# Kernel optimization log

Hardware: AMD Instinct MI355X
Metric: run time of the kernel (lower is better)

Reference implementation:

```python
import jax, jax.numpy as jnp
import numpy as np

B, S, H, E, V = 32, 256, 512, 300, 32000
ALEN, LLEN, POL = 4, 16, 3
HOP, LAM = 10, 0.01


def _layernorm(x, g, b, eps=1e-12):
    mu = jnp.mean(x, -1, keepdims=True)
    var = jnp.mean((x - mu) ** 2, -1, keepdims=True)
    return (x - mu) / jnp.sqrt(var + eps) * g + b


def _pos_weight(x, a0, a1, text_len, aspect_len):
    # vectorized version of ASGCN_NEW.position_weight
    j = jnp.arange(x.shape[1])[None, :]
    cl = (text_len - aspect_len).astype(jnp.float32)[:, None]
    a0b, a1b, tlb = a0[:, None], a1[:, None], text_len[:, None]
    w = jnp.where(j < a0b, 1.0 - (a0b - j) / cl,
        jnp.where(j <= a1b, 0.0,
        jnp.where(j < tlb, 1.0 - (j - a1b) / cl, 0.0)))
    return w[:, :, None] * x


def _mask(x, a0, a1):
    j = jnp.arange(x.shape[1])[None, :]
    m = ((j >= a0[:, None]) & (j <= a1[:, None])).astype(x.dtype)
    return m[:, :, None] * x


def _gcn(x, adj, w, b):
    h = jnp.einsum('bsh,hk->bsk', x, w)
    denom = jnp.sum(adj, 2, keepdims=True) + 1.0
    return jnp.einsum('bst,bth->bsh', adj, h) / denom + b


def _conv1d(x, w, b):
    # x: [B,S,C] -> conv over S with kernel 3, pad 1 -> [B,S,C]
    y = jax.lax.conv_general_dilated(jnp.swapaxes(x, 1, 2), w, (1,), ((1, 1),),
                                     dimension_numbers=('NCH', 'OIH', 'NCH'))
    return jnp.swapaxes(y + b[None, :, None], 1, 2)


def _lstm_dir(x, mask, wih, whh, b, reverse):
    # masked LSTM matching pack_padded semantics: state frozen / output zero at pad
    xs = jnp.swapaxes(x, 0, 1)       # [S,B,E]
    ms = jnp.swapaxes(mask, 0, 1)    # [S,B] bool
    if reverse:
        xs, ms = xs[::-1], ms[::-1]
    pre = jnp.einsum('sbe,ge->sbg', xs, wih) + b
    h0 = jnp.zeros((x.shape[0], whh.shape[1]), x.dtype)

    def step(carry, inp):
        h, c = carry
        p, m = inp
        g = p + h @ whh.T
        i, f, gg, o = jnp.split(g, 4, -1)
        c_new = jax.nn.sigmoid(f) * c + jax.nn.sigmoid(i) * jnp.tanh(gg)
        h_new = jax.nn.sigmoid(o) * jnp.tanh(c_new)
        m_ = m[:, None]
        return (jnp.where(m_, h_new, h), jnp.where(m_, c_new, c)), jnp.where(m_, h_new, 0.0)

    _, ys = jax.lax.scan(step, (h0, h0), (pre, ms))
    if reverse:
        ys = ys[::-1]
    return jnp.swapaxes(ys, 0, 1)


def _hop_attend(m, text_out, g, b):
    tT = jnp.swapaxes(text_out, 1, 2)
    for _ in range(HOP - 1):
        alpha = jnp.einsum('bsh,bht->bst', m, tT)          # [B,S,S]
        a = jnp.einsum('bst,bth->bsh', alpha, text_out)    # [B,S,H]
        m = LAM * _layernorm(jax.nn.sigmoid(a), g, b) + m
    alpha_mat = jnp.einsum('bsh,bht->bst', m, tT)
    alpha = jax.nn.softmax(jnp.sum(alpha_mat, 1, keepdims=True), axis=2)  # [B,1,S]
    return jnp.einsum('bot,bth->boh', alpha, text_out)[:, 0]              # [B,H]


def setup_inputs() -> dict:
    key = jax.random.key(0)
    ks = jax.random.split(key, 20)
    sc = 0.05
    text_indices = jax.random.randint(ks[0], (B, S), 1, V)
    aspect_indices = jax.random.randint(ks[1], (B, ALEN), 1, V)
    left_indices = jax.random.randint(ks[2], (B, LLEN), 1, V)
    adj = (jax.random.uniform(ks[3], (B, S, S)) < 0.1).astype(jnp.float32)
    adj = jnp.minimum(adj + jnp.eye(S, dtype=jnp.float32)[None], 1.0)
    return {
        'text_indices': text_indices,
        'aspect_indices': aspect_indices,
        'left_indices': left_indices,
        'adj': adj,
        'embedding': jax.random.normal(ks[4], (V, E)) * sc,
        'lstm_wih_f': jax.random.normal(ks[5], (4 * H, E)) * sc,
        'lstm_whh_f': jax.random.normal(ks[6], (4 * H, H)) * sc,
        'lstm_b_f': jnp.zeros((4 * H,), jnp.float32),
        'lstm_wih_b': jax.random.normal(ks[7], (4 * H, E)) * sc,
        'lstm_whh_b': jax.random.normal(ks[8], (4 * H, H)) * sc,
        'lstm_b_b': jnp.zeros((4 * H,), jnp.float32),
        'gc_w': jax.random.normal(ks[9], (6, H, H)) * sc,
        'gc_b': jnp.zeros((6, H), jnp.float32),
        'conv1_w': jax.random.normal(ks[10], (H, H, 3)) * sc,
        'conv1_b': jnp.zeros((H,), jnp.float32),
        'conv2_w': jax.random.normal(ks[11], (H, H, 3)) * sc,
        'conv2_b': jnp.zeros((H,), jnp.float32),
        'fc2_w': jax.random.normal(ks[12], (POL, 3 * H)) * sc,
        'fc2_b': jnp.zeros((POL,), jnp.float32),
        'ln_g': jnp.ones((3, H), jnp.float32),
        'ln_b': jnp.zeros((3, H), jnp.float32),
    }


def _forward(text_indices, aspect_indices, left_indices, adj, embedding,
             lstm_wih_f, lstm_whh_f, lstm_b_f, lstm_wih_b, lstm_whh_b, lstm_b_b,
             gc_w, gc_b, conv1_w, conv1_b, conv2_w, conv2_b, fc2_w, fc2_b, ln_g, ln_b):
    text_len = jnp.sum(text_indices != 0, -1)
    aspect_len = jnp.sum(aspect_indices != 0, -1)
    left_len = jnp.sum(left_indices != 0, -1)
    a0 = left_len
    a1 = left_len + aspect_len - 1
    text = embedding[text_indices]  # dropout identity in eval mode
    m = text_indices != 0
    hf = _lstm_dir(text, m, lstm_wih_f, lstm_whh_f, lstm_b_f, False)
    hb = _lstm_dir(text, m, lstm_wih_b, lstm_whh_b, lstm_b_b, True)
    # concat fwd/bwd then reshape(B,S,H,2).mean(-1), exactly as the torch code
    text_out = jnp.concatenate([hf, hb], -1).reshape(B, S, H, 2).mean(-1)

    pw = lambda t: _pos_weight(t, a0, a1, text_len, aspect_len)

    x_conv = jax.nn.relu(_conv1d(pw(text_out), conv1_w, conv1_b))
    x_conv = jax.nn.relu(_conv1d(pw(x_conv), conv2_w, conv2_b))

    x = jax.nn.relu(_gcn(pw(text_out), adj, gc_w[0], gc_b[0]))
    pwx = pw(x)
    graph_mask = jnp.zeros_like(x)
    for k in range(1, 6):
        graph_mask = graph_mask + _mask(jax.nn.relu(_gcn(pwx, adj, gc_w[k], gc_b[k])), a0, a1)

    a1_vec = _hop_attend(graph_mask, text_out, ln_g[0], ln_b[0])
    a2_vec = _hop_attend(_mask(text_out, a0, a1), text_out, ln_g[1], ln_b[1])
    a3_vec = _hop_attend(_mask(x_conv, a0, a1), text_out, ln_g[2], ln_b[2])

    fnout = jnp.concatenate([a1_vec, a2_vec, a3_vec], 1)  # [B, 3H]
    return fnout @ fc2_w.T + fc2_b


def reference(text_indices, aspect_indices, left_indices, adj, embedding,
              lstm_wih_f, lstm_whh_f, lstm_b_f, lstm_wih_b, lstm_whh_b, lstm_b_b,
              gc_w, gc_b, conv1_w, conv1_b, conv2_w, conv2_b, fc2_w, fc2_b, ln_g, ln_b):
    return _forward(text_indices, aspect_indices, left_indices, adj, embedding,
                    lstm_wih_f, lstm_whh_f, lstm_b_f, lstm_wih_b, lstm_whh_b, lstm_b_b,
                    gc_w, gc_b, conv1_w, conv1_b, conv2_w, conv2_b, fc2_w, fc2_b, ln_g, ln_b)
```

## Files before the change

kernel.cpp:

```cpp
#include <hip/hip_runtime.h>
#include <hip/hip_fp16.h>

typedef unsigned int u32;
typedef unsigned long long u64;

static constexpr size_t OFF_X2    = 0;
static constexpr size_t OFF_PRE   = 9830400;
static constexpr size_t OFF_MB    = 131072;
static constexpr size_t OFF_CNT   = 133120;
static constexpr size_t OFF_TOUT  = 0;
static constexpr size_t OFF_TOUTT = 16777216;
static constexpr size_t OFF_PWT   = 33554432;
static constexpr size_t OFF_AGG0  = 50331648;
static constexpr size_t OFF_Y     = 76939264;
static constexpr size_t OFF_PWX   = 110493696;
static constexpr size_t OFF_WD    = 127270912;
static constexpr size_t OFF_WIH   = 131465216;
static constexpr size_t OFF_BIA   = 136380416;
static constexpr size_t OFF_W1T   = 136396800;
static constexpr size_t OFF_W2T   = 139542528;
static constexpr size_t OFF_META  = 142688256;
static constexpr size_t OFF_CLF   = 142688768;
static constexpr size_t OFF_DEN   = 142688896;
static constexpr size_t OFF_POSW  = 142721664;
static constexpr size_t OFF_AGGM  = 142754432;
static constexpr size_t OFF_GMSK  = 143016576;
static constexpr size_t OFF_C1PW  = 143278720;
static constexpr size_t OFF_XC2   = 143671936;
static constexpr size_t OFF_AVEC  = 143934080;
static constexpr size_t WS_NEED   = 144130688;

__device__ __forceinline__ float sigf(float x) { return 1.f / (1.f + expf(-x)); }

typedef _Float16 half8 __attribute__((ext_vector_type(8)));
typedef float f32x4 __attribute__((ext_vector_type(4)));
union U4H8 { uint4 u; half8 h; };

__global__ void len_k(const int* __restrict__ ti, const int* __restrict__ ai,
                      const int* __restrict__ li, int* __restrict__ meta, float* __restrict__ clf)
{
    int b = threadIdx.x;
    if (b >= 32) return;
    int tl = 0;
    for (int s = 0; s < 256; ++s) tl += (ti[b*256+s] != 0);
    int al = 0;
    for (int i = 0; i < 4; ++i) al += (ai[b*4+i] != 0);
    int ll = 0;
    for (int i = 0; i < 16; ++i) ll += (li[b*16+i] != 0);
    meta[b]      = ll;
    meta[32+b]   = ll + al - 1;
    meta[64+b]   = al;
    meta[96+b]   = tl;
    clf[b] = (float)(tl - al);
}

__global__ __launch_bounds__(256)
void pd_k(const float* __restrict__ adj, const int* __restrict__ meta,
          const float* __restrict__ clf, float* __restrict__ denom, float* __restrict__ posw)
{
    int row = blockIdx.x;
    int b = row >> 8, s = row & 255;
    int tid = threadIdx.x;
    float v = adj[(size_t)row*256 + tid];
    #pragma unroll
    for (int off = 1; off < 64; off <<= 1) v += __shfl_xor(v, off);
    __shared__ float rd[4];
    if ((tid & 63) == 0) rd[tid >> 6] = v;
    __syncthreads();
    if (tid == 0) {
        denom[row] = rd[0] + rd[1] + rd[2] + rd[3] + 1.f;
        int a0 = meta[b], a1 = meta[32+b], tl = meta[96+b];
        float cl = clf[b];
        float w;
        if (s < a0)       w = 1.f - (float)(a0 - s) / cl;
        else if (s <= a1) w = 0.f;
        else if (s < tl)  w = 1.f - (float)(s - a1) / cl;
        else              w = 0.f;
        posw[row] = w;
    }
}

__global__ __launch_bounds__(128)
void gather_k(const int* __restrict__ ti, const float* __restrict__ emb, __half* __restrict__ X2h)
{
    int row = blockIdx.x;
    int b = row & 31, s = row >> 5;
    int idx = ti[b*256 + s];
    const float* e = emb + (size_t)idx*300;
    __half* o = X2h + (size_t)row*320;
    for (int k = threadIdx.x; k < 320; k += 128)
        o[k] = (k < 300) ? __float2half(e[k]) : __ushort_as_half((unsigned short)0);
}

__global__ __launch_bounds__(256)
void wpackih_k(const float* __restrict__ wf, const float* __restrict__ wb, u32* __restrict__ Wih)
{
    u32 idx = blockIdx.x*256 + threadIdx.x;
    if (idx >= 655360u) return;
    int n = idx / 160;
    int j = idx - n*160;
    int k0 = 2*j;
    const float* w = (n < 2048) ? (wf + (size_t)n*300) : (wb + (size_t)(n - 2048)*300);
    float v0 = (k0   < 300) ? w[k0]   : 0.f;
    float v1 = (k0+1 < 300) ? w[k0+1] : 0.f;
    Wih[idx] = (u32)__half_as_ushort(__float2half(v0)) |
               ((u32)__half_as_ushort(__float2half(v1)) << 16);
}

__global__ __launch_bounds__(256)
void wmf_k(const float* __restrict__ wf, const float* __restrict__ wb, u32* __restrict__ Wmf)
{
    u32 idx = blockIdx.x*256 + threadIdx.x;
    int e2 = idx & 3;
    int l  = (idx >> 2) & 63;
    int c  = (idx >> 8) & 3;
    int mt = (idx >> 10) & 1;
    int wv = (idx >> 11) & 3;
    int g  = (idx >> 13) & 63;
    int dir = (int)(idx >> 19);
    int kloc = wv*128 + c*32 + 16*(e2 >> 1) + 4*(l >> 4) + 2*(e2 & 1);
    int ml = mt*16 + (l & 15);
    int n = (ml & 3)*512 + g*8 + (ml >> 2);
    const float* w = dir ? wb : wf;
    float v0 = w[(size_t)n*512 + kloc];
    float v1 = w[(size_t)n*512 + kloc + 1];
    Wmf[idx] = (u32)__half_as_ushort(__float2half(v0)) |
               ((u32)__half_as_ushort(__float2half(v1)) << 16);
}

__global__ void maskb_k(const int* __restrict__ ti, u32* __restrict__ mb)
{
    int s = threadIdx.x;
    u32 w = 0;
    for (int b = 0; b < 32; ++b) w |= (u32)(ti[b*256 + s] != 0) << b;
    mb[s] = w;
}

__global__ __launch_bounds__(256)
void wtrans_k(const float* __restrict__ w1, const float* __restrict__ w2,
              float* __restrict__ w1T, float* __restrict__ w2T)
{
    u32 idx = blockIdx.x*256 + threadIdx.x;
    const float* src = blockIdx.y ? w2 : w1;
    float* dst = blockIdx.y ? w2T : w1T;
    int k = idx >> 18;
    int i = (idx >> 9) & 511;
    int o = idx & 511;
    dst[idx] = src[((size_t)o*512 + i)*3 + k];
}

__global__ __launch_bounds__(256)
void pre_mfma_k(const u32* __restrict__ X2u, const u32* __restrict__ Wihu,
                const float* __restrict__ bias, __half* __restrict__ pre)
{
    __shared__ u32 As2[16*132];
    __shared__ u32 Bs2[16*132];
    const int tid = threadIdx.x;
    const int wv = tid >> 6;
    const int l  = tid & 63;
    const int q  = l >> 4;
    const int l15 = l & 15;
    const int wm = wv & 1, wn = wv >> 1;
    const int m0 = blockIdx.x * 128;
    const int n0 = blockIdx.y * 128;

    f32x4 acc[4][4];
    #pragma unroll
    for (int mt = 0; mt < 4; ++mt)
        #pragma unroll
        for (int nt = 0; nt < 4; ++nt)
            acc[mt][nt] = (f32x4){0.f, 0.f, 0.f, 0.f};

    const int srow = tid >> 4;
    const int sj   = tid & 15;

    for (int kb = 0; kb < 10; ++kb) {
        #pragma unroll
        for (int i = 0; i < 8; ++i) {
            int row = srow + i*16;
            As2[sj*132 + row] = X2u[(size_t)(m0 + row)*160 + kb*16 + sj];
            Bs2[sj*132 + row] = Wihu[(size_t)(n0 + row)*160 + kb*16 + sj];
        }
        __syncthreads();

        U4H8 bf[4];
        #pragma unroll
        for (int nt = 0; nt < 4; ++nt) {
            int col = wn*64 + nt*16 + l15;
            bf[nt].u = make_uint4(Bs2[(2*q)*132 + col], Bs2[(2*q+1)*132 + col],
                                  Bs2[(2*q+8)*132 + col], Bs2[(2*q+9)*132 + col]);
        }
        #pragma unroll
        for (int mt = 0; mt < 4; ++mt) {
            int row = wm*64 + mt*16 + l15;
            U4H8 af;
            af.u = make_uint4(As2[(2*q)*132 + row], As2[(2*q+1)*132 + row],
                              As2[(2*q+8)*132 + row], As2[(2*q+9)*132 + row]);
            #pragma unroll
            for (int nt = 0; nt < 4; ++nt)
                acc[mt][nt] = __builtin_amdgcn_mfma_f32_16x16x32_f16(af.h, bf[nt].h, acc[mt][nt], 0, 0, 0);
        }
        __syncthreads();
    }

    #pragma unroll
    for (int nt = 0; nt < 4; ++nt) {
        int col = n0 + wn*64 + nt*16 + l15;
        float bv = bias[col];
        #pragma unroll
        for (int mt = 0; mt < 4; ++mt) {
            int rbase = m0 + wm*64 + mt*16 + q*4;
            #pragma unroll
            for (int p = 0; p < 4; ++p)
                pre[(size_t)(rbase + p)*4096 + col] = __float2half(acc[mt][nt][p] + bv);
        }
    }
}

__global__ __launch_bounds__(256, 1)
void lstm_scan5_k(const __half* __restrict__ pre, const u32* __restrict__ Wmf,
                  const u32* __restrict__ mb, float* __restrict__ y,
                  u32* __restrict__ cnt, u64* __restrict__ Hs)
{
    __shared__ u32 hs[32*264];
    __shared__ float gred[4352];

    const int tid = threadIdx.x;
    const int wv = tid >> 6;
    const int l  = tid & 63;
    const int q  = l >> 4;
    const int l15 = l & 15;
    const int dir = blockIdx.x & 1;
    const int g   = blockIdx.x >> 1;
    const int b2 = tid >> 3;
    const int jj = tid & 7;
    const int gcol = g*8 + jj;

    half8 afr[2][4];
    {
        const uint4* wp = (const uint4*)(Wmf + ((((size_t)dir*64 + g)*4 + wv)*2048)) + l;
        #pragma unroll
        for (int mt = 0; mt < 2; ++mt)
            #pragma unroll
            for (int c = 0; c < 4; ++c)
                afr[mt][c] = __builtin_bit_cast(half8, wp[(mt*4 + c)*64]);
    }

    float hreg = 0.f, creg = 0.f;

    const int s0 = dir ? 255 : 0;
    __half ph[4];
    #pragma unroll
    for (int gt = 0; gt < 4; ++gt)
        ph[gt] = pre[((size_t)s0*32 + b2)*4096 + dir*2048 + gt*512 + gcol];
    u32 mbv = mb[s0];

    const int ks64 = wv*64;
    const int srow = tid >> 3, scol = tid & 7;

    for (int t = 0; t < 256; ++t) {
        const int s = dir ? (255 - t) : t;

        __half phn[4];
        #pragma unroll
        for (int gt = 0; gt < 4; ++gt) phn[gt] = ph[gt];
        u32 mbn = mbv;
        if (t < 255) {
            int sn = dir ? (254 - t) : (t + 1);
            #pragma unroll
            for (int gt = 0; gt < 4; ++gt)
                phn[gt] = pre[((size_t)sn*32 + b2)*4096 + dir*2048 + gt*512 + gcol];
            mbn = mb[sn];
        }

        if (t == 0) {
            u32* dst = &hs[srow*264 + scol*4];
            #pragma unroll
            for (int i = 0; i < 8; ++i) *(uint4*)(dst + i*32) = make_uint4(0u,0u,0u,0u);
        } else {
            if (tid == 0) {
                const u32* cpp = cnt + (size_t)t*2 + dir;
                int guard = 0;
                while (__hip_atomic_load(cpp, __ATOMIC_RELAXED, __HIP_MEMORY_SCOPE_AGENT) < 64u) {
                    __builtin_amdgcn_s_sleep(2);
                    if (++guard > (1 << 22)) break;
                }
            }
            __syncthreads();
            int bi = (int)(__brev((u32)t) >> 24);
            const uint4* src = (const uint4*)(Hs + ((size_t)(bi*2 + dir)*32)*128);
            const uint4* tp = src + srow*64 + scol;
            uint4 vv[8];
            #pragma unroll
            for (int i = 0; i < 8; ++i) vv[i] = tp[i*8];
            u32* dst = &hs[srow*264 + scol*4];
            #pragma unroll
            for (int i = 0; i < 8; ++i) *(uint4*)(dst + i*32) = vv[i];
        }
        __syncthreads();

        f32x4 acc[2][2];
        #pragma unroll
        for (int mt = 0; mt < 2; ++mt)
            #pragma unroll
            for (int nt = 0; nt < 2; ++nt)
                acc[mt][nt] = (f32x4){0.f, 0.f, 0.f, 0.f};
        #pragma unroll
        for (int c = 0; c < 4; ++c) {
            #pragma unroll
            for (int nt = 0; nt < 2; ++nt) {
                int base = (nt*16 + l15)*264 + ks64 + c*16 + 2*q;
                uint4 bw = make_uint4(hs[base], hs[base+1], hs[base+8], hs[base+9]);
                half8 bfr = __builtin_bit_cast(half8, bw);
                acc[0][nt] = __builtin_amdgcn_mfma_f32_16x16x32_f16(afr[0][c], bfr, acc[0][nt], 0, 0, 0);
                acc[1][nt] = __builtin_amdgcn_mfma_f32_16x16x32_f16(afr[1][c], bfr, acc[1][nt], 0, 0, 0);
            }
        }

        #pragma unroll
        for (int mt = 0; mt < 2; ++mt)
            #pragma unroll
            for (int nt = 0; nt < 2; ++nt)
                #pragma unroll
                for (int p = 0; p < 4; ++p)
                    gred[(((wv*2 + mt)*2 + nt)*16 + q*4 + p)*17 + l15] = acc[mt][nt][p];
        __syncthreads();

        float gv[4];
        #pragma unroll
        for (int gt = 0; gt < 4; ++gt) {
            int ml = 4*jj + gt;
            int mt = ml >> 4, r = ml & 15;
            int ntile = b2 >> 4, n = b2 & 15;
            float sum = 0.f;
            #pragma unroll
            for (int w2 = 0; w2 < 4; ++w2)
                sum += gred[(((w2*2 + mt)*2 + ntile)*16 + r)*17 + n];
            gv[gt] = sum + __half2float(ph[gt]);
        }
        float cn = sigf(gv[1])*creg + sigf(gv[0])*tanhf(gv[2]);
        float hn = sigf(gv[3])*tanhf(cn);
        bool mk = (mbv >> b2) & 1u;
        if (mk) { hreg = hn; creg = cn; }

        {
            int l4 = l & ~3;
            float h0 = __shfl(hreg, l4 + 0);
            float h1 = __shfl(hreg, l4 + 1);
            float h2 = __shfl(hreg, l4 + 2);
            float h3 = __shfl(hreg, l4 + 3);
            if ((tid & 3) == 0) {
                u32 lo = (u32)__half_as_ushort(__float2half(h0)) |
                         ((u32)__half_as_ushort(__float2half(h1)) << 16);
                u32 hi = (u32)__half_as_ushort(__float2half(h2)) |
                         ((u32)__half_as_ushort(__float2half(h3)) << 16);
                u64 pk = (u64)lo | ((u64)hi << 32);
                int bi2 = (int)(__brev((u32)(t + 1)) >> 24);
                int wsel = (tid >> 2) & 1;
                __hip_atomic_store(&Hs[((size_t)(bi2*2 + dir)*32 + b2)*128 + 2*g + wsel], pk,
                                   __ATOMIC_RELAXED, __HIP_MEMORY_SCOPE_AGENT);
            }
        }
        asm volatile("s_waitcnt vmcnt(0)" ::: "memory");
        __syncthreads();
        if (tid == 0) {
            __hip_atomic_fetch_add(cnt + (size_t)(t + 1)*2 + dir, 1u,
                                   __ATOMIC_RELAXED, __HIP_MEMORY_SCOPE_AGENT);
        }
        y[(((size_t)dir*32 + b2)*256 + s)*512 + gcol] = mk ? hn : 0.f;

        mbv = mbn;
        #pragma unroll
        for (int gt = 0; gt < 4; ++gt) ph[gt] = phn[gt];
    }
}

__global__ __launch_bounds__(256)
void combine_k(const float* __restrict__ y, const float* __restrict__ posw,
               float* __restrict__ text_out, float* __restrict__ pw_text)
{
    size_t idx = (size_t)blockIdx.x*256 + threadIdx.x;
    int hh = (int)(idx & 511);
    size_t rem = idx >> 9;
    int s = (int)(rem & 255);
    int b = (int)(rem >> 8);
    const float* p;
    if (hh < 256) p = y + (((size_t)b*256 + s)*512 + 2*hh);
    else          p = y + (((size_t)(32 + b)*256 + s)*512 + 2*(hh - 256));
    float v = 0.5f*(p[0] + p[1]);
    text_out[idx] = v;
    pw_text[idx] = v * posw[b*256 + s];
}

__global__ __launch_bounds__(256)
void transp_k(const float* __restrict__ text_out, float* __restrict__ tOutT)
{
    __shared__ float tile[32][33];
    int b = blockIdx.z, s0 = blockIdx.x*32, h0 = blockIdx.y*32;
    int tx = threadIdx.x & 31, ty4 = threadIdx.x >> 5;
    #pragma unroll
    for (int rr = 0; rr < 4; ++rr) {
        int sy = ty4 + rr*8;
        tile[sy][tx] = text_out[((size_t)b*256 + s0 + sy)*512 + h0 + tx];
    }
    __syncthreads();
    #pragma unroll
    for (int rr = 0; rr < 4; ++rr) {
        int hy = ty4 + rr*8;
        tOutT[((size_t)b*512 + h0 + hy)*256 + s0 + tx] = tile[tx][hy];
    }
}

template<int MODE, bool BT>
__global__ __launch_bounds__(256)
void gemm_k(const float* __restrict__ A, const float* __restrict__ B,
            void* __restrict__ C, int M, int N, int K,
            long sA, long sB, long sC,
            const float* __restrict__ bias,
            const float* __restrict__ denom,
            const float* __restrict__ posw)
{
    __shared__ float As[32][132];
    __shared__ float Bs[32][132];
    const int z = blockIdx.z;
    A += (size_t)z * sA;
    B += (size_t)z * sB;
    const int m0 = blockIdx.x * 128;
    const int n0 = blockIdx.y * 128;
    const int tid = threadIdx.x;
    const int tx = tid & 15, ty = tid >> 4;
    float acc[8][8];
    #pragma unroll
    for (int i = 0; i < 8; ++i)
        #pragma unroll
        for (int j = 0; j < 8; ++j) acc[i][j] = 0.f;
    const int nkb = (K + 31) >> 5;
    for (int kb = 0; kb < nkb; ++kb) {
        const int k0 = kb << 5;
        #pragma unroll
        for (int rep = 0; rep < 4; ++rep) {
            int idx = rep*256 + tid;
            int row = idx >> 3;
            int c4 = (idx & 7) << 2;
            int gk = k0 + c4;
            const float* ap = A + (size_t)(m0 + row)*K + gk;
            float4 v;
            if (gk + 3 < K) v = *(const float4*)ap;
            else {
                v.x = (gk   < K) ? ap[0] : 0.f;
                v.y = (gk+1 < K) ? ap[1] : 0.f;
                v.z = (gk+2 < K) ? ap[2] : 0.f;
                v.w = (gk+3 < K) ? ap[3] : 0.f;
            }
            As[c4+0][row] = v.x; As[c4+1][row] = v.y;
            As[c4+2][row] = v.z; As[c4+3][row] = v.w;
        }
        if (BT) {
            #pragma unroll
            for (int rep = 0; rep < 4; ++rep) {
                int idx = rep*256 + tid;
                int row = idx >> 3;
                int c4 = (idx & 7) << 2;
                int gk = k0 + c4;
                const float* bp = B + (size_t)(n0 + row)*K + gk;
                float4 v;
                if (gk + 3 < K) v = *(const float4*)bp;
                else {
                    v.x = (gk   < K) ? bp[0] : 0.f;
                    v.y = (gk+1 < K) ? bp[1] : 0.f;
                    v.z = (gk+2 < K) ? bp[2] : 0.f;
                    v.w = (gk+3 < K) ? bp[3] : 0.f;
                }
                Bs[c4+0][row] = v.x; Bs[c4+1][row] = v.y;
                Bs[c4+2][row] = v.z; Bs[c4+3][row] = v.w;
            }
        } else {
            #pragma unroll
            for (int rep = 0; rep < 4; ++rep) {
                int idx = rep*256 + tid;
                int kk = idx >> 5;
                int nn = (idx & 31) << 2;
                int gk = k0 + kk;
                float4 v = make_float4(0.f, 0.f, 0.f, 0.f);
                if (gk < K) v = *(const float4*)(B + (size_t)gk*N + n0 + nn);
                *(float4*)&Bs[kk][nn] = v;
            }
        }
        __syncthreads();
        #pragma unroll
        for (int k = 0; k < 32; ++k) {
            float a[8], br[8];
            *(float4*)&a[0]  = *(const float4*)&As[k][ty*8];
            *(float4*)&a[4]  = *(const float4*)&As[k][ty*8+4];
            *(float4*)&br[0] = *(const float4*)&Bs[k][tx*8];
            *(float4*)&br[4] = *(const float4*)&Bs[k][tx*8+4];
            #pragma unroll
            for (int i = 0; i < 8; ++i)
                #pragma unroll
                for (int j = 0; j < 8; ++j)
                    acc[i][j] = fmaf(a[i], br[j], acc[i][j]);
        }
        __syncthreads();
    }
    if (MODE == 1) {
        float* cp = (float*)C + (size_t)z*sC;
        #pragma unroll
        for (int i = 0; i < 8; ++i) {
            size_t ro = (size_t)(m0 + ty*8 + i)*N + n0 + tx*8;
            *(float4*)(cp + ro)     = make_float4(acc[i][0], acc[i][1], acc[i][2], acc[i][3]);
            *(float4*)(cp + ro + 4) = make_float4(acc[i][4], acc[i][5], acc[i][6], acc[i][7]);
        }
    } else {
        float* cp = (float*)C + (size_t)z*sC;
        #pragma unroll
        for (int i = 0; i < 8; ++i) {
            int m = m0 + ty*8 + i;
            float inv = 1.f / denom[m];
            float pw = posw[m];
            size_t ro = (size_t)m*N + n0 + tx*8;
            #pragma unroll
            for (int j = 0; j < 8; ++j) {
                float v = fmaf(acc[i][j], inv, bias[n0 + tx*8 + j]);
                cp[ro + j] = fmaxf(v, 0.f) * pw;
            }
        }
    }
}

__global__ __launch_bounds__(256)
void aggm_k(const float* __restrict__ adj, const float* __restrict__ pwx,
            const int* __restrict__ meta, float* __restrict__ aggm)
{
    int b = blockIdx.x >> 2, r = blockIdx.x & 3;
    int a0 = meta[b], nm = meta[64+b];
    int s = a0 + r; if (s > 255) s = 255;
    __shared__ float arow[256];
    int tid = threadIdx.x;
    arow[tid] = adj[((size_t)b*256 + s)*256 + tid];
    __syncthreads();
    float acc0 = 0.f, acc1 = 0.f;
    for (int t = 0; t < 256; ++t) {
        float av = arow[t];
        acc0 = fmaf(av, pwx[((size_t)b*256 + t)*512 + tid], acc0);
        acc1 = fmaf(av, pwx[((size_t)b*256 + t)*512 + tid + 256], acc1);
    }
    bool ok = (r < nm);
    aggm[((size_t)b*4 + r)*512 + tid]       = ok ? acc0 : 0.f;
    aggm[((size_t)b*4 + r)*512 + tid + 256] = ok ? acc1 : 0.f;
}

__global__ __launch_bounds__(256)
void gmaskn_k(const float* __restrict__ aggm, const float* __restrict__ gcw,
              const float* __restrict__ gcb, const int* __restrict__ meta,
              const float* __restrict__ denom, float* __restrict__ gmsk)
{
    int b = blockIdx.x >> 1, hf = blockIdx.x & 1;
    int col = hf*256 + threadIdx.x;
    int a0 = meta[b], nm = meta[64+b];
    __shared__ float rows[4][512];
    int tid = threadIdx.x;
    #pragma unroll
    for (int r = 0; r < 4; ++r) {
        rows[r][tid]       = aggm[((size_t)b*4 + r)*512 + tid];
        rows[r][tid + 256] = aggm[((size_t)b*4 + r)*512 + tid + 256];
    }
    float inv[4];
    #pragma unroll
    for (int r = 0; r < 4; ++r) {
        int srow = a0 + r; if (srow > 255) srow = 255;
        inv[r] = 1.f / denom[b*256 + srow];
    }
    __syncthreads();
    float gm[4] = {0.f, 0.f, 0.f, 0.f};
    for (int k = 1; k <= 5; ++k) {
        const float* w = gcw + (size_t)k*262144 + col;
        float bb = gcb[k*512 + col];
        float ak[4] = {0.f, 0.f, 0.f, 0.f};
        for (int c = 0; c < 512; ++c) {
            float wv = w[(size_t)c*512];
            #pragma unroll
            for (int r = 0; r < 4; ++r) ak[r] = fmaf(rows[r][c], wv, ak[r]);
        }
        #pragma unroll
        for (int r = 0; r < 4; ++r) gm[r] += fmaxf(fmaf(ak[r], inv[r], bb), 0.f);
    }
    #pragma unroll
    for (int r = 0; r < 4; ++r)
        gmsk[((size_t)b*4 + r)*512 + col] = (r < nm) ? gm[r] : 0.f;
}

__global__ __launch_bounds__(256)
void conv1n_k(const float* __restrict__ pwt, const float* __restrict__ w1T,
              const float* __restrict__ b1, const int* __restrict__ meta,
              const float* __restrict__ posw, float* __restrict__ c1pw)
{
    int b = blockIdx.x >> 1, hf = blockIdx.x & 1;
    int col = hf*256 + threadIdx.x;
    int a0 = meta[b];
    __shared__ float rows[8][512];
    int tid = threadIdx.x;
    #pragma unroll
    for (int i = 0; i < 8; ++i) {
        int si = a0 - 2 + i;
        bool v = (si >= 0 && si < 256);
        rows[i][tid]       = v ? pwt[((size_t)b*256 + si)*512 + tid]       : 0.f;
        rows[i][tid + 256] = v ? pwt[((size_t)b*256 + si)*512 + tid + 256] : 0.f;
    }
    __syncthreads();
    float bv = b1[col];
    float acc[6] = {bv, bv, bv, bv, bv, bv};
    #pragma unroll
    for (int kk = 0; kk < 3; ++kk) {
        const float* w = w1T + (size_t)kk*262144 + col;
        for (int c = 0; c < 512; ++c) {
            float wv = w[(size_t)c*512];
            #pragma unroll
            for (int r = 0; r < 6; ++r) acc[r] = fmaf(rows[r + kk][c], wv, acc[r]);
        }
    }
    #pragma unroll
    for (int r = 0; r < 6; ++r) {
        int s = a0 - 1 + r;
        bool valid = (s >= 0 && s < 256);
        float pv = valid ? posw[b*256 + s] : 0.f;
        c1pw[((size_t)b*6 + r)*512 + col] = valid ? fmaxf(acc[r], 0.f)*pv : 0.f;
    }
}

__global__ __launch_bounds__(256)
void conv2n_k(const float* __restrict__ c1pw, const float* __restrict__ w2T,
              const float* __restrict__ b2, const int* __restrict__ meta,
              float* __restrict__ xc2)
{
    int b = blockIdx.x >> 1, hf = blockIdx.x & 1;
    int col = hf*256 + threadIdx.x;
    int nm = meta[64+b];
    __shared__ float rows[6][512];
    int tid = threadIdx.x;
    #pragma unroll
    for (int i = 0; i < 6; ++i) {
        rows[i][tid]       = c1pw[((size_t)b*6 + i)*512 + tid];
        rows[i][tid + 256] = c1pw[((size_t)b*6 + i)*512 + tid + 256];
    }
    __syncthreads();
    float bv = b2[col];
    float acc[4] = {bv, bv, bv, bv};
    #pragma unroll
    for (int kk = 0; kk < 3; ++kk) {
        const float* w = w2T + (size_t)kk*262144 + col;
        for (int c = 0; c < 512; ++c) {
            float wv = w[(size_t)c*512];
            #pragma unroll
            for (int r = 0; r < 4; ++r) acc[r] = fmaf(rows[r + kk][c], wv, acc[r]);
        }
    }
    #pragma unroll
    for (int r = 0; r < 4; ++r)
        xc2[((size_t)b*4 + r)*512 + col] = (r < nm) ? fmaxf(acc[r], 0.f) : 0.f;
}

__global__ __launch_bounds__(512)
void attend_k(const float* __restrict__ text_out, const float* __restrict__ tOutT,
              const float* __restrict__ gmsk, const float* __restrict__ xc2,
              const int* __restrict__ meta,
              const float* __restrict__ lng, const float* __restrict__ lnb,
              float* __restrict__ avec)
{
    __shared__ float m5[5][512];
    __shared__ float alpha[5][256];
    __shared__ float apart[5][256];
    __shared__ float wt[256];
    __shared__ float msum[512];
    __shared__ float red[8];
    int b = blockIdx.x, att = blockIdx.y;
    int tid = threadIdx.x;
    int a0 = meta[b], nm = meta[64+b];
    #pragma unroll
    for (int r = 0; r < 4; ++r) {
        float v = 0.f;
        if (r < nm) {
            if (att == 0)      v = gmsk[((size_t)b*4 + r)*512 + tid];
            else if (att == 1) v = text_out[((size_t)b*256 + a0 + r)*512 + tid];
            else               v = xc2[((size_t)b*4 + r)*512 + tid];
        }
        m5[r][tid] = v;
    }
    m5[4][tid] = 0.f;
    const float* tT = tOutT + (size_t)b*512*256;
    const float* tO = text_out + (size_t)b*256*512;
    float lgam = lng[att*512 + tid], lbet = lnb[att*512 + tid];
    __syncthreads();
    for (int hop = 0; hop < 9; ++hop) {
        {
            int t = tid & 255, hf = tid >> 8;
            float a5[5] = {0.f, 0.f, 0.f, 0.f, 0.f};
            const float* tp = tT + (size_t)(hf*256)*256 + t;
            for (int h = 0; h < 256; ++h) {
                float v = tp[(size_t)h*256];
                int hh = hf*256 + h;
                #pragma unroll
                for (int r = 0; r < 5; ++r) a5[r] = fmaf(m5[r][hh], v, a5[r]);
            }
            if (hf == 0) { for (int r = 0; r < 5; ++r) alpha[r][t] = a5[r]; }
            else         { for (int r = 0; r < 5; ++r) apart[r][t] = a5[r]; }
        }
        __syncthreads();
        for (int idx = tid; idx < 1280; idx += 512) {
            int r = idx >> 8, t2 = idx & 255;
            alpha[r][t2] += apart[r][t2];
        }
        __syncthreads();
        float a5[5] = {0.f, 0.f, 0.f, 0.f, 0.f};
        for (int t = 0; t < 256; ++t) {
            float v = tO[(size_t)t*512 + tid];
            #pragma unroll
            for (int r = 0; r < 5; ++r) a5[r] = fmaf(alpha[r][t], v, a5[r]);
        }
        #pragma unroll 1
        for (int r = 0; r < 5; ++r) {
            float xv = sigf(a5[r]);
            float s1 = xv;
            #pragma unroll
            for (int off = 1; off < 64; off <<= 1) s1 += __shfl_xor(s1, off);
            if ((tid & 63) == 0) red[tid >> 6] = s1;
            __syncthreads();
            float mu = (red[0]+red[1]+red[2]+red[3]+red[4]+red[5]+red[6]+red[7]) * (1.f/512.f);
            __syncthreads();
            float d = xv - mu;
            float s2 = d*d;
            #pragma unroll
            for (int off = 1; off < 64; off <<= 1) s2 += __shfl_xor(s2, off);
            if ((tid & 63) == 0) red[tid >> 6] = s2;
            __syncthreads();
            float var = (red[0]+red[1]+red[2]+red[3]+red[4]+red[5]+red[6]+red[7]) * (1.f/512.f);
            __syncthreads();
            float ln = d * rsqrtf(var + 1e-12f) * lgam + lbet;
            if (r < nm || r == 4) m5[r][tid] += 0.01f * ln;
        }
        __syncthreads();
    }
    {
        float ms = 0.f;
        #pragma unroll
        for (int r = 0; r < 4; ++r) if (r < nm) ms += m5[r][tid];
        ms += (float)(256 - nm) * m5[4][tid];
        msum[tid] = ms;
    }
    __syncthreads();
    {
        int t = tid & 255, hf = tid >> 8;
        float sc = 0.f;
        const float* tp = tT + (size_t)(hf*256)*256 + t;
        for (int h = 0; h < 256; ++h) sc = fmaf(msum[hf*256 + h], tp[(size_t)h*256], sc);
        if (hf == 0) alpha[0][t] = sc; else apart[0][t] = sc;
    }
    __syncthreads();
    float sv = (tid < 256) ? (alpha[0][tid] + apart[0][tid]) : -3.0e38f;
    float mx = sv;
    #pragma unroll
    for (int off = 1; off < 64; off <<= 1) mx = fmaxf(mx, __shfl_xor(mx, off));
    if ((tid & 63) == 0) red[tid >> 6] = mx;
    __syncthreads();
    mx = fmaxf(fmaxf(fmaxf(red[0], red[1]), fmaxf(red[2], red[3])),
               fmaxf(fmaxf(red[4], red[5]), fmaxf(red[6], red[7])));
    __syncthreads();
    float ex = (tid < 256) ? expf(sv - mx) : 0.f;
    float ss = ex;
    #pragma unroll
    for (int off = 1; off < 64; off <<= 1) ss += __shfl_xor(ss, off);
    if ((tid & 63) == 0) red[tid >> 6] = ss;
    __syncthreads();
    float tot = red[0]+red[1]+red[2]+red[3]+red[4]+red[5]+red[6]+red[7];
    __syncthreads();
    if (tid < 256) wt[tid] = ex / tot;
    __syncthreads();
    float acc = 0.f;
    for (int t = 0; t < 256; ++t) acc = fmaf(wt[t], tO[(size_t)t*512 + tid], acc);
    avec[((size_t)att*32 + b)*512 + tid] = acc;
}

__global__ __launch_bounds__(128)
void final_k(const float* __restrict__ avec, const float* __restrict__ fw,
             const float* __restrict__ fbb, float* __restrict__ out)
{
    int b = blockIdx.x, tid = threadIdx.x;
    float a0 = 0.f, a1 = 0.f, a2 = 0.f;
    for (int j = tid; j < 1536; j += 128) {
        float v = avec[((size_t)(j >> 9)*32 + b)*512 + (j & 511)];
        a0 = fmaf(v, fw[j], a0);
        a1 = fmaf(v, fw[1536 + j], a1);
        a2 = fmaf(v, fw[3072 + j], a2);
    }
    #pragma unroll
    for (int off = 1; off < 64; off <<= 1) {
        a0 += __shfl_xor(a0, off); a1 += __shfl_xor(a1, off); a2 += __shfl_xor(a2, off);
    }
    __shared__ float red[6];
    if ((tid & 63) == 0) { int w = tid >> 6; red[w] = a0; red[2+w] = a1; red[4+w] = a2; }
    __syncthreads();
    if (tid == 0) {
        out[b*3+0] = red[0] + red[1] + fbb[0];
        out[b*3+1] = red[2] + red[3] + fbb[1];
        out[b*3+2] = red[4] + red[5] + fbb[2];
    }
}

extern "C" void kernel_launch(void* const* d_in, const int* in_sizes, int n_in,
                              void* d_out, int out_size, void* d_ws, size_t ws_size,
                              hipStream_t stream)
{
    (void)in_sizes; (void)n_in; (void)out_size;
    if (ws_size < WS_NEED) return;
    const int*   ti    = (const int*)d_in[0];
    const int*   ai    = (const int*)d_in[1];
    const int*   li    = (const int*)d_in[2];
    const float* adj   = (const float*)d_in[3];
    const float* emb   = (const float*)d_in[4];
    const float* wih_f = (const float*)d_in[5];
    const float* whh_f = (const float*)d_in[6];
    const float* b_f   = (const float*)d_in[7];
    const float* wih_b = (const float*)d_in[8];
    const float* whh_b = (const float*)d_in[9];
    const float* b_b   = (const float*)d_in[10];
    const float* gcw   = (const float*)d_in[11];
    const float* gcb   = (const float*)d_in[12];
    const float* c1w   = (const float*)d_in[13];
    const float* c1b   = (const float*)d_in[14];
    const float* c2w   = (const float*)d_in[15];
    const float* c2b   = (const float*)d_in[16];
    const float* fw    = (const float*)d_in[17];
    const float* fb    = (const float*)d_in[18];
    const float* lng   = (const float*)d_in[19];
    const float* lnb   = (const float*)d_in[20];

    char* ws = (char*)d_ws;
    __half* X2h      = (__half*)(ws + OFF_X2);
    __half* pre      = (__half*)(ws + OFF_PRE);
    u32*    mb       = (u32*)(ws + OFF_MB);
    u32*    cnt      = (u32*)(ws + OFF_CNT);
    float*  text_out = (float*)(ws + OFF_TOUT);
    float*  tOutT    = (float*)(ws + OFF_TOUTT);
    float*  pw_text  = (float*)(ws + OFF_PWT);
    float*  agg0     = (float*)(ws + OFF_AGG0);
    float*  y        = (float*)(ws + OFF_Y);
    float*  pwx      = (float*)(ws + OFF_PWX);
    u64*    Hs       = (u64*)(ws + OFF_PWX);
    u32*    Wmf      = (u32*)(ws + OFF_WD);
    u32*    Wih      = (u32*)(ws + OFF_WIH);
    float*  biascat  = (float*)(ws + OFF_BIA);
    float*  w1T      = (float*)(ws + OFF_W1T);
    float*  w2T      = (float*)(ws + OFF_W2T);
    int*    meta     = (int*)(ws + OFF_META);
    float*  clf      = (float*)(ws + OFF_CLF);
    float*  denom    = (float*)(ws + OFF_DEN);
    float*  posw     = (float*)(ws + OFF_POSW);
    float*  aggm     = (float*)(ws + OFF_AGGM);
    float*  gmsk     = (float*)(ws + OFF_GMSK);
    float*  c1pw     = (float*)(ws + OFF_C1PW);
    float*  xc2      = (float*)(ws + OFF_XC2);
    float*  avec     = (float*)(ws + OFF_AVEC);

    len_k<<<1, 64, 0, stream>>>(ti, ai, li, meta, clf);
    pd_k<<<8192, 256, 0, stream>>>(adj, meta, clf, denom, posw);
    gather_k<<<8192, 128, 0, stream>>>(ti, emb, X2h);
    wpackih_k<<<2560, 256, 0, stream>>>(wih_f, wih_b, Wih);
    wmf_k<<<4096, 256, 0, stream>>>(whh_f, whh_b, Wmf);
    wtrans_k<<<dim3(3072, 2), 256, 0, stream>>>(c1w, c2w, w1T, w2T);
    hipMemcpyAsync(biascat,        b_f, 2048*4, hipMemcpyDeviceToDevice, stream);
    hipMemcpyAsync(biascat + 2048, b_b, 2048*4, hipMemcpyDeviceToDevice, stream);

    pre_mfma_k<<<dim3(64, 32), 256, 0, stream>>>((const u32*)X2h, Wih, biascat, pre);

    maskb_k<<<1, 256, 0, stream>>>(ti, mb);
    hipMemsetAsync(cnt, 0, (size_t)257*2*4, stream);

    lstm_scan5_k<<<128, 256, 0, stream>>>(pre, Wmf, mb, y, cnt, Hs);
    combine_k<<<16384, 256, 0, stream>>>(y, posw, text_out, pw_text);
    transp_k<<<dim3(8, 16, 32), 256, 0, stream>>>(text_out, tOutT);

    gemm_k<1, false><<<dim3(2, 4, 32), 256, 0, stream>>>(adj, pw_text, (void*)agg0,
        256, 512, 256, 65536L, 131072L, 131072L, nullptr, nullptr, nullptr);
    gemm_k<2, false><<<dim3(64, 4, 1), 256, 0, stream>>>(agg0, gcw, (void*)pwx,
        8192, 512, 512, 0, 0, 0, gcb, denom, posw);

    aggm_k<<<128, 256, 0, stream>>>(adj, pwx, meta, aggm);
    gmaskn_k<<<64, 256, 0, stream>>>(aggm, gcw, gcb, meta, denom, gmsk);
    conv1n_k<<<64, 256, 0, stream>>>(pw_text, w1T, c1b, meta, posw, c1pw);
    conv2n_k<<<64, 256, 0, stream>>>(c1pw, w2T, c2b, meta, xc2);
    attend_k<<<dim3(32, 3), 512, 0, stream>>>(text_out, tOutT, gmsk, xc2, meta, lng, lnb, avec);
    final_k<<<32, 128, 0, stream>>>(avec, fw, fb, (float*)d_out);
}
```

Measured before the change: 1.734 ms.

## Replace atomic counter barrier with per-block flags polled by a full wavefront

The cross-block step barrier in the LSTM scan now uses one flag per producer block per timestep instead of a single fetch-add counter. Each producer writes its own flag with a plain atomic store, and a whole wavefront of 64 lanes polls the 64 flags, combined with __all. This removes contention from atomic adds on a single word and uses a shorter sleep. The prefetch of the next step's pre-activations and mask moves to the end of the step. That shortens the live range of the prefetched values, but the load overlaps less with the barrier wait. The flag buffer is larger and needs a larger memset.

```diff
diff --git a/kernel.cpp b/kernel.cpp
--- a/kernel.cpp
+++ b/kernel.cpp
@@ -7,7 +7,7 @@
 static constexpr size_t OFF_X2    = 0;
 static constexpr size_t OFF_PRE   = 9830400;
 static constexpr size_t OFF_MB    = 131072;
-static constexpr size_t OFF_CNT   = 133120;
+static constexpr size_t OFF_FLG   = 135168;
 static constexpr size_t OFF_TOUT  = 0;
 static constexpr size_t OFF_TOUTT = 16777216;
 static constexpr size_t OFF_PWT   = 33554432;
@@ -218,9 +218,9 @@
 }
 
 __global__ __launch_bounds__(256, 1)
-void lstm_scan5_k(const __half* __restrict__ pre, const u32* __restrict__ Wmf,
+void lstm_scan6_k(const __half* __restrict__ pre, const u32* __restrict__ Wmf,
                   const u32* __restrict__ mb, float* __restrict__ y,
-                  u32* __restrict__ cnt, u64* __restrict__ Hs)
+                  u32* __restrict__ flags, u64* __restrict__ Hs)
 {
     __shared__ u32 hs[32*264];
     __shared__ float gred[4352];
@@ -261,28 +261,18 @@
     for (int t = 0; t < 256; ++t) {
         const int s = dir ? (255 - t) : t;
 
-        __half phn[4];
-        #pragma unroll
-        for (int gt = 0; gt < 4; ++gt) phn[gt] = ph[gt];
-        u32 mbn = mbv;
-        if (t < 255) {
-            int sn = dir ? (254 - t) : (t + 1);
-            #pragma unroll
-            for (int gt = 0; gt < 4; ++gt)
-                phn[gt] = pre[((size_t)sn*32 + b2)*4096 + dir*2048 + gt*512 + gcol];
-            mbn = mb[sn];
-        }
-
         if (t == 0) {
             u32* dst = &hs[srow*264 + scol*4];
             #pragma unroll
             for (int i = 0; i < 8; ++i) *(uint4*)(dst + i*32) = make_uint4(0u,0u,0u,0u);
         } else {
-            if (tid == 0) {
-                const u32* cpp = cnt + (size_t)t*2 + dir;
+            if (tid < 64) {
+                const u32* fp = flags + (size_t)t*128 + dir*64 + tid;
                 int guard = 0;
-                while (__hip_atomic_load(cpp, __ATOMIC_RELAXED, __HIP_MEMORY_SCOPE_AGENT) < 64u) {
-                    __builtin_amdgcn_s_sleep(2);
+                u32 fv = __hip_atomic_load(fp, __ATOMIC_RELAXED, __HIP_MEMORY_SCOPE_AGENT);
+                while (!__all(fv != 0u)) {
+                    __builtin_amdgcn_s_sleep(1);
+                    fv = __hip_atomic_load(fp, __ATOMIC_RELAXED, __HIP_MEMORY_SCOPE_AGENT);
                     if (++guard > (1 << 22)) break;
                 }
             }
@@ -364,14 +354,18 @@
         asm volatile("s_waitcnt vmcnt(0)" ::: "memory");
         __syncthreads();
         if (tid == 0) {
-            __hip_atomic_fetch_add(cnt + (size_t)(t + 1)*2 + dir, 1u,
-                                   __ATOMIC_RELAXED, __HIP_MEMORY_SCOPE_AGENT);
+            __hip_atomic_store(flags + (size_t)(t + 1)*128 + dir*64 + g, 1u,
+                               __ATOMIC_RELAXED, __HIP_MEMORY_SCOPE_AGENT);
         }
         y[(((size_t)dir*32 + b2)*256 + s)*512 + gcol] = mk ? hn : 0.f;
 
-        mbv = mbn;
-        #pragma unroll
-        for (int gt = 0; gt < 4; ++gt) ph[gt] = phn[gt];
+        if (t < 255) {
+            int sn = dir ? (254 - t) : (t + 1);
+            #pragma unroll
+            for (int gt = 0; gt < 4; ++gt)
+                ph[gt] = pre[((size_t)sn*32 + b2)*4096 + dir*2048 + gt*512 + gcol];
+            mbv = mb[sn];
+        }
     }
 }
 
@@ -837,7 +831,7 @@
     __half* X2h      = (__half*)(ws + OFF_X2);
     __half* pre      = (__half*)(ws + OFF_PRE);
     u32*    mb       = (u32*)(ws + OFF_MB);
-    u32*    cnt      = (u32*)(ws + OFF_CNT);
+    u32*    flags    = (u32*)(ws + OFF_FLG);
     float*  text_out = (float*)(ws + OFF_TOUT);
     float*  tOutT    = (float*)(ws + OFF_TOUTT);
     float*  pw_text  = (float*)(ws + OFF_PWT);
@@ -872,9 +866,9 @@
     pre_mfma_k<<<dim3(64, 32), 256, 0, stream>>>((const u32*)X2h, Wih, biascat, pre);
 
     maskb_k<<<1, 256, 0, stream>>>(ti, mb);
-    hipMemsetAsync(cnt, 0, (size_t)257*2*4, stream);
-
-    lstm_scan5_k<<<128, 256, 0, stream>>>(pre, Wmf, mb, y, cnt, Hs);
+    hipMemsetAsync(flags, 0, (size_t)257*128*4, stream);
+
+    lstm_scan6_k<<<128, 256, 0, stream>>>(pre, Wmf, mb, y, flags, Hs);
     combine_k<<<16384, 256, 0, stream>>>(y, posw, text_out, pw_text);
     transp_k<<<dim3(8, 16, 32), 256, 0, stream>>>(text_out, tOutT);
 
```

After: 1.607 ms. 7.3% less time.
